# Performance work log

Measured on AMD Instinct MI355X. Metric: run time of the kernel, lower is better.

Reference implementation:

```python
import jax, jax.numpy as jnp
import numpy as np

B, S, D, UNITS = 4, 512, 256, 128
NEG = -1e9


def setup_inputs() -> dict:
    key = jax.random.key(0)
    k1, k2, k3, k4 = jax.random.split(key, 4)
    values = jax.random.normal(k1, (B, S, D), dtype=jnp.float32)
    Wq = jax.random.normal(k2, (D, UNITS), dtype=jnp.float32) * (1.0 / np.sqrt(D))
    Wv = jax.random.normal(k3, (D, UNITS), dtype=jnp.float32) * (1.0 / np.sqrt(D))
    Vw = jax.random.normal(k4, (UNITS,), dtype=jnp.float32) * (1.0 / np.sqrt(UNITS))
    return {"values": values, "Wq": Wq, "Wv": Wv, "Vw": Vw}


def reference(values, Wq, Wv, Vw):
    # values: [B, S, D]
    query = values @ Wq            # [B, S, U]
    value = values @ Wv            # [B, S, U]
    # additive (Bahdanau) score: V . tanh(q_i + v_j) -> [B, S, S]
    feat = jnp.tanh(query[:, :, None, :] + value[:, None, :, :])  # [B,S,S,U]
    score = jnp.einsum('biju,u->bij', feat, Vw)
    seq_len = values.shape[1]
    causal = jnp.tril(jnp.ones((seq_len, seq_len), dtype=jnp.float32))  # lower-tri = visible
    score = score + (1.0 - causal)[None, :, :] * jnp.asarray(NEG, score.dtype)
    attn = jax.nn.softmax(score, axis=-1)          # [B, S, S]
    context = jnp.matmul(attn, values)             # [B, S, D]
    return context
```

## Files before the change

kernel.cpp:

```cpp
#include <hip/hip_runtime.h>
#include <hip/hip_fp16.h>

#define SEQ 512
#define DIM 256
#define UN  128
#define BSZ 2048
#define CSC 2.8853900817779268f
#define EVS 2176
#define VTS 2176
#define PS  640

typedef _Float16 half8 __attribute__((ext_vector_type(8)));
typedef float   float4v __attribute__((ext_vector_type(4)));
struct h4s { __half2 a, b; };

static __device__ __forceinline__ unsigned short f2bf(float x) {
  unsigned u = __float_as_uint(x);
  u += 0x7FFF + ((u >> 16) & 1);
  return (unsigned short)(u >> 16);
}
static __device__ __forceinline__ float bf2f(unsigned short s) {
  return __uint_as_float((unsigned)s << 16);
}
static __device__ __forceinline__ float rdlane(float v, int k) {
  return __int_as_float(__builtin_amdgcn_readlane(__float_as_int(v), k));
}

__global__ __launch_bounds__(256) void proj_kernel(
    const float* __restrict__ values, const float* __restrict__ Wq,
    const float* __restrict__ Wv, float* __restrict__ Eq,
    unsigned short* __restrict__ Ev, _Float16* __restrict__ Vt) {
  __shared__ float vsm[4 * DIM];
  const int t = threadIdx.x;
  const int r0 = blockIdx.x * 4;
  {
    const int row = t >> 6, c4 = (t & 63) * 4;
    const float4 v = *(const float4*)(values + (r0 + row) * DIM + c4);
    *(float4*)&vsm[row * DIM + c4] = v;
  }
  __syncthreads();
  {
    h4s o;
    o.a = __floats2half2_rn(vsm[0 * DIM + t], vsm[1 * DIM + t]);
    o.b = __floats2half2_rn(vsm[2 * DIM + t], vsm[3 * DIM + t]);
    *(h4s*)(Vt + (size_t)t * VTS + r0) = o;
  }
  const int half = t >> 7, u = t & 127;
  const float* __restrict__ W = half ? Wv : Wq;
  float acc[4] = {0.f, 0.f, 0.f, 0.f};
  for (int d = 0; d < DIM; d += 4) {
    const float w0 = W[(d + 0) * UN + u], w1 = W[(d + 1) * UN + u];
    const float w2 = W[(d + 2) * UN + u], w3 = W[(d + 3) * UN + u];
#pragma unroll
    for (int k = 0; k < 4; ++k) {
      const float4 v = *(const float4*)&vsm[k * DIM + d];
      acc[k] = fmaf(v.x, w0, acc[k]);
      acc[k] = fmaf(v.y, w1, acc[k]);
      acc[k] = fmaf(v.z, w2, acc[k]);
      acc[k] = fmaf(v.w, w3, acc[k]);
    }
  }
  if (!half) {
#pragma unroll
    for (int k = 0; k < 4; ++k)
      Eq[(r0 + k) * UN + u] = __builtin_amdgcn_exp2f(acc[k] * CSC);
  } else {
    ushort4 o;
    o.x = f2bf(__builtin_amdgcn_exp2f(acc[0] * CSC));
    o.y = f2bf(__builtin_amdgcn_exp2f(acc[1] * CSC));
    o.z = f2bf(__builtin_amdgcn_exp2f(acc[2] * CSC));
    o.w = f2bf(__builtin_amdgcn_exp2f(acc[3] * CSC));
    *(ushort4*)(Ev + (size_t)u * EVS + r0) = o;
  }
}

__global__ __launch_bounds__(256, 4) void score_kernel(
    const float* __restrict__ Eq, const unsigned short* __restrict__ Ev,
    const float* __restrict__ Vw, _Float16* __restrict__ P) {
  __shared__ float sc[2 * SEQ];
  __shared__ float scp[2 * SEQ];
  __shared__ float invs[2];

  const int t = threadIdx.x;
  const int x = blockIdx.x;
  const int b = x >> 8, p = x & 255;
  const int bS = b * SEQ;
  const int i = p;
  const int ihi = SEQ - 1 - p;
  const int jhi = ihi;

  const float* __restrict__ eql = Eq + (size_t)(bS + i) * UN;
  const float* __restrict__ eqh = Eq + (size_t)(bS + ihi) * UN;

  {
    const int flip = ((x ^ (x >> 1) ^ (x >> 8)) & 1) << 6;
    const int tt = t ^ flip;
    const int lane = t & 63;
    const int qd = tt & 127, jb = qd << 2;
    const int u0 = (tt >> 7) << 6;
    float* __restrict__ so = (tt >> 7) ? scp : sc;
    const unsigned short* __restrict__ evp = Ev + (size_t)u0 * EVS + bS + jb;
    const float qhv = eqh[u0 + lane];
    const float qlv = eql[u0 + lane];
    const float wvv = Vw[u0 + lane];
#define LDE(K) (*(const ushort4*)(evp + (size_t)(K) * EVS))
    if ((tt & 64) == 0) {
      float h0=0.f,h1=0.f,h2=0.f,h3=0.f,l0=0.f,l1=0.f,l2=0.f,l3=0.f;
      ushort4 e[4] = {LDE(0), LDE(1), LDE(2), LDE(3)};
#pragma clang loop unroll(disable)
      for (int k = 0; k < 64; k += 4) {
#pragma unroll
        for (int r = 0; r < 4; ++r) {
          const ushort4 n = LDE(k + 4 + r);
          const float qh = rdlane(qhv, k + r);
          const float ql = rdlane(qlv, k + r);
          const float ww = rdlane(wvv, k + r);
          const float f0 = bf2f(e[r].x), f1 = bf2f(e[r].y);
          const float f2 = bf2f(e[r].z), f3 = bf2f(e[r].w);
          const float a0 = fmaf(ql, f0, 1.f), b0 = fmaf(qh, f0, 1.f);
          const float a1 = fmaf(ql, f1, 1.f), b1 = fmaf(qh, f1, 1.f);
          const float a2 = fmaf(ql, f2, 1.f), b2 = fmaf(qh, f2, 1.f);
          const float a3 = fmaf(ql, f3, 1.f), b3 = fmaf(qh, f3, 1.f);
          const float s0 = ww * __builtin_amdgcn_rcpf(a0 * b0);
          const float s1 = ww * __builtin_amdgcn_rcpf(a1 * b1);
          const float s2 = ww * __builtin_amdgcn_rcpf(a2 * b2);
          const float s3 = ww * __builtin_amdgcn_rcpf(a3 * b3);
          l0 = fmaf(s0, b0, l0); h0 = fmaf(s0, a0, h0);
          l1 = fmaf(s1, b1, l1); h1 = fmaf(s1, a1, h1);
          l2 = fmaf(s2, b2, l2); h2 = fmaf(s2, a2, h2);
          l3 = fmaf(s3, b3, l3); h3 = fmaf(s3, a3, h3);
          e[r] = n;
        }
      }
      *(float4*)&so[SEQ + jb] = make_float4(h0, h1, h2, h3);
      *(float4*)&so[jb]       = make_float4(l0, l1, l2, l3);
    } else if (jb <= jhi) {
      float h0=0.f,h1=0.f,h2=0.f,h3=0.f;
      ushort4 e[4] = {LDE(0), LDE(1), LDE(2), LDE(3)};
#pragma clang loop unroll(disable)
      for (int k = 0; k < 64; k += 4) {
#pragma unroll
        for (int r = 0; r < 4; ++r) {
          const ushort4 n = LDE(k + 4 + r);
          const float q  = rdlane(qhv, k + r);
          const float ww = rdlane(wvv, k + r);
          const float f0 = bf2f(e[r].x), f1 = bf2f(e[r].y);
          const float f2 = bf2f(e[r].z), f3 = bf2f(e[r].w);
          const float a  = fmaf(q, f0, 1.f), bb = fmaf(q, f1, 1.f);
          const float c  = fmaf(q, f2, 1.f), d  = fmaf(q, f3, 1.f);
          const float sA = ww * __builtin_amdgcn_rcpf(a * bb);
          const float sB = ww * __builtin_amdgcn_rcpf(c * d);
          h0 = fmaf(sA, bb, h0); h1 = fmaf(sA, a, h1);
          h2 = fmaf(sB, d,  h2); h3 = fmaf(sB, c, h3);
          e[r] = n;
        }
      }
      *(float4*)&so[SEQ + jb] = make_float4(h0, h1, h2, h3);
    }
#undef LDE
  }
  __syncthreads();

  {
    const int w = t >> 6, l = t & 63;
    if (w < 2) {
      const int jmax = (w == 0) ? i : jhi;
      float* __restrict__ r0p = sc + w * SEQ;
      const float* __restrict__ r1p = scp + w * SEQ;
      float m = 1e30f;
      for (int j = l; j <= jmax; j += 64) m = fminf(m, r0p[j] + r1p[j]);
#pragma unroll
      for (int o = 32; o; o >>= 1) m = fminf(m, __shfl_xor(m, o));
      float sum = 0.f;
      for (int j = l; j <= jmax; j += 64) {
        const float pr = __builtin_amdgcn_exp2f((m - (r0p[j] + r1p[j])) * CSC);
        r0p[j] = pr;
        sum += pr;
      }
#pragma unroll
      for (int o = 32; o; o >>= 1) sum += __shfl_xor(sum, o);
      if (l == 0) invs[w] = __builtin_amdgcn_rcpf(sum);
    }
  }
  __syncthreads();

  {
    const float invLo = invs[0], invHi = invs[1];
    const int t2 = t + 256;
    const float pLo = (t <= i) ? sc[t] * invLo : 0.f;
    const float pHa = sc[SEQ + t] * invHi;
    const float pHb = (t2 <= jhi) ? sc[SEQ + t2] * invHi : 0.f;
    P[(size_t)(bS + i) * PS + t]    = (_Float16)pLo;
    P[(size_t)(bS + ihi) * PS + t]  = (_Float16)pHa;
    P[(size_t)(bS + ihi) * PS + t2] = (_Float16)pHb;
  }
}

__global__ __launch_bounds__(256) void ctx_kernel(
    const _Float16* __restrict__ P, const _Float16* __restrict__ Vt,
    float* __restrict__ out) {
  const int t = threadIdx.x, lane = t & 63, g = t >> 6;
  const int x = blockIdx.x;
  const int b = x >> 7, ri = (x >> 2) & 31, cg = x & 3;
  const int bS = b * SEQ;
  const int d0 = cg * 64 + g * 16;
  const int m = lane & 15, q = lane >> 4;
  const int Kmax = 16 * ri + 16;

  const _Float16* __restrict__ pA = P  + (size_t)(bS + 16 * ri + m) * PS + q * 8;
  const _Float16* __restrict__ pB = Vt + (size_t)(d0 + m) * VTS + bS + q * 8;
  float4v acc = {0.f, 0.f, 0.f, 0.f};
  for (int k0 = 0; k0 < Kmax; k0 += 32) {
    const half8 a  = *(const half8*)(pA + k0);
    const half8 bv = *(const half8*)(pB + k0);
    acc = __builtin_amdgcn_mfma_f32_16x16x32_f16(a, bv, acc, 0, 0, 0);
  }
  float* __restrict__ o = out + (size_t)(bS + 16 * ri + q * 4) * DIM + d0 + m;
#pragma unroll
  for (int r = 0; r < 4; ++r) o[(size_t)r * DIM] = acc[r];
}

extern "C" void kernel_launch(void* const* d_in, const int* in_sizes, int n_in,
                              void* d_out, int out_size, void* d_ws, size_t ws_size,
                              hipStream_t stream) {
  const float* values = (const float*)d_in[0];
  const float* Wq     = (const float*)d_in[1];
  const float* Wv     = (const float*)d_in[2];
  const float* Vw     = (const float*)d_in[3];
  float* out = (float*)d_out;
  float* Eq = (float*)d_ws;
  unsigned short* Ev = (unsigned short*)(Eq + (size_t)BSZ * UN);
  _Float16* Vt = (_Float16*)(Ev + (size_t)136 * EVS);
  _Float16* P  = Vt + (size_t)DIM * VTS;
  proj_kernel<<<dim3(BSZ / 4), 256, 0, stream>>>(values, Wq, Wv, Eq, Ev, Vt);
  score_kernel<<<dim3(4 * 256), 256, 0, stream>>>(Eq, Ev, Vw, P);
  ctx_kernel<<<dim3(4 * 32 * 4), 256, 0, stream>>>(P, Vt, out);
}
```

Before: 99.71 us.

## Split score and softmax into separate kernels with finer score parallelism

Restructures the score stage so each block handles half the key range and waves split the unit dimension, reducing partials via shared memory and writing raw scores to a global buffer. A new softmax kernel reads rows, applies the causal mask, normalizes, and writes fp16 probabilities. This removes the serialized, mostly idle softmax phase inside the score kernel and raises occupancy, at the cost of an extra launch, a global round trip for scores, and some wasted computation on masked columns.

```diff
diff --git a/kernel.cpp b/kernel.cpp
--- a/kernel.cpp
+++ b/kernel.cpp
@@ -74,126 +74,120 @@
   }
 }
 
-__global__ __launch_bounds__(256, 4) void score_kernel(
+__global__ __launch_bounds__(256, 8) void score2_kernel(
     const float* __restrict__ Eq, const unsigned short* __restrict__ Ev,
-    const float* __restrict__ Vw, _Float16* __restrict__ P) {
-  __shared__ float sc[2 * SEQ];
-  __shared__ float scp[2 * SEQ];
-  __shared__ float invs[2];
-
-  const int t = threadIdx.x;
+    const float* __restrict__ Vw, float* __restrict__ Sd) {
+  __shared__ float pl[4 * 256];
+  __shared__ float ph[4 * 256];
+  const int t = threadIdx.x, lane = t & 63, w = t >> 6;
   const int x = blockIdx.x;
-  const int b = x >> 8, p = x & 255;
+  const int pairIdx = x >> 1, jhalf = x & 1;
+  const int b = pairIdx >> 8, p = pairIdx & 255;
   const int bS = b * SEQ;
-  const int i = p;
-  const int ihi = SEQ - 1 - p;
-  const int jhi = ihi;
-
-  const float* __restrict__ eql = Eq + (size_t)(bS + i) * UN;
-  const float* __restrict__ eqh = Eq + (size_t)(bS + ihi) * UN;
-
-  {
-    const int flip = ((x ^ (x >> 1) ^ (x >> 8)) & 1) << 6;
-    const int tt = t ^ flip;
-    const int lane = t & 63;
-    const int qd = tt & 127, jb = qd << 2;
-    const int u0 = (tt >> 7) << 6;
-    float* __restrict__ so = (tt >> 7) ? scp : sc;
-    const unsigned short* __restrict__ evp = Ev + (size_t)u0 * EVS + bS + jb;
-    const float qhv = eqh[u0 + lane];
-    const float qlv = eql[u0 + lane];
-    const float wvv = Vw[u0 + lane];
+  const int i = p, ihi = SEQ - 1 - p;
+  const int u0 = w << 5;
+  const int jb = lane << 2;
+
+  const int lk = lane & 31;
+  const float qlv = Eq[(size_t)(bS + i) * UN + u0 + lk];
+  const float qhv = Eq[(size_t)(bS + ihi) * UN + u0 + lk];
+  const float wvv = Vw[u0 + lk];
+
+  const unsigned short* __restrict__ evp =
+      Ev + (size_t)u0 * EVS + bS + (jhalf << 8) + jb;
 #define LDE(K) (*(const ushort4*)(evp + (size_t)(K) * EVS))
-    if ((tt & 64) == 0) {
-      float h0=0.f,h1=0.f,h2=0.f,h3=0.f,l0=0.f,l1=0.f,l2=0.f,l3=0.f;
-      ushort4 e[4] = {LDE(0), LDE(1), LDE(2), LDE(3)};
+  if (jhalf == 0) {
+    float h0=0.f,h1=0.f,h2=0.f,h3=0.f,l0=0.f,l1=0.f,l2=0.f,l3=0.f;
+    ushort4 e[4] = {LDE(0), LDE(1), LDE(2), LDE(3)};
 #pragma clang loop unroll(disable)
-      for (int k = 0; k < 64; k += 4) {
-#pragma unroll
-        for (int r = 0; r < 4; ++r) {
-          const ushort4 n = LDE(k + 4 + r);
-          const float qh = rdlane(qhv, k + r);
-          const float ql = rdlane(qlv, k + r);
-          const float ww = rdlane(wvv, k + r);
-          const float f0 = bf2f(e[r].x), f1 = bf2f(e[r].y);
-          const float f2 = bf2f(e[r].z), f3 = bf2f(e[r].w);
-          const float a0 = fmaf(ql, f0, 1.f), b0 = fmaf(qh, f0, 1.f);
-          const float a1 = fmaf(ql, f1, 1.f), b1 = fmaf(qh, f1, 1.f);
-          const float a2 = fmaf(ql, f2, 1.f), b2 = fmaf(qh, f2, 1.f);
-          const float a3 = fmaf(ql, f3, 1.f), b3 = fmaf(qh, f3, 1.f);
-          const float s0 = ww * __builtin_amdgcn_rcpf(a0 * b0);
-          const float s1 = ww * __builtin_amdgcn_rcpf(a1 * b1);
-          const float s2 = ww * __builtin_amdgcn_rcpf(a2 * b2);
-          const float s3 = ww * __builtin_amdgcn_rcpf(a3 * b3);
-          l0 = fmaf(s0, b0, l0); h0 = fmaf(s0, a0, h0);
-          l1 = fmaf(s1, b1, l1); h1 = fmaf(s1, a1, h1);
-          l2 = fmaf(s2, b2, l2); h2 = fmaf(s2, a2, h2);
-          l3 = fmaf(s3, b3, l3); h3 = fmaf(s3, a3, h3);
-          e[r] = n;
-        }
+    for (int k = 0; k < 32; k += 4) {
+#pragma unroll
+      for (int r = 0; r < 4; ++r) {
+        const ushort4 n = LDE(k + 4 + r);
+        const float qh = rdlane(qhv, k + r);
+        const float ql = rdlane(qlv, k + r);
+        const float ww = rdlane(wvv, k + r);
+        const float f0 = bf2f(e[r].x), f1 = bf2f(e[r].y);
+        const float f2 = bf2f(e[r].z), f3 = bf2f(e[r].w);
+        const float a0 = fmaf(ql, f0, 1.f), b0 = fmaf(qh, f0, 1.f);
+        const float a1 = fmaf(ql, f1, 1.f), b1 = fmaf(qh, f1, 1.f);
+        const float a2 = fmaf(ql, f2, 1.f), b2 = fmaf(qh, f2, 1.f);
+        const float a3 = fmaf(ql, f3, 1.f), b3 = fmaf(qh, f3, 1.f);
+        const float s0 = ww * __builtin_amdgcn_rcpf(a0 * b0);
+        const float s1 = ww * __builtin_amdgcn_rcpf(a1 * b1);
+        const float s2 = ww * __builtin_amdgcn_rcpf(a2 * b2);
+        const float s3 = ww * __builtin_amdgcn_rcpf(a3 * b3);
+        l0 = fmaf(s0, b0, l0); h0 = fmaf(s0, a0, h0);
+        l1 = fmaf(s1, b1, l1); h1 = fmaf(s1, a1, h1);
+        l2 = fmaf(s2, b2, l2); h2 = fmaf(s2, a2, h2);
+        l3 = fmaf(s3, b3, l3); h3 = fmaf(s3, a3, h3);
+        e[r] = n;
       }
-      *(float4*)&so[SEQ + jb] = make_float4(h0, h1, h2, h3);
-      *(float4*)&so[jb]       = make_float4(l0, l1, l2, l3);
-    } else if (jb <= jhi) {
-      float h0=0.f,h1=0.f,h2=0.f,h3=0.f;
-      ushort4 e[4] = {LDE(0), LDE(1), LDE(2), LDE(3)};
+    }
+    *(float4*)&pl[(w << 8) + jb] = make_float4(l0, l1, l2, l3);
+    *(float4*)&ph[(w << 8) + jb] = make_float4(h0, h1, h2, h3);
+    __syncthreads();
+    const float lo = pl[t] + pl[256 + t] + pl[512 + t] + pl[768 + t];
+    const float hi = ph[t] + ph[256 + t] + ph[512 + t] + ph[768 + t];
+    Sd[(size_t)(bS + i) * SEQ + t]   = lo;
+    Sd[(size_t)(bS + ihi) * SEQ + t] = hi;
+  } else {
+    float h0=0.f,h1=0.f,h2=0.f,h3=0.f;
+    ushort4 e[4] = {LDE(0), LDE(1), LDE(2), LDE(3)};
 #pragma clang loop unroll(disable)
-      for (int k = 0; k < 64; k += 4) {
-#pragma unroll
-        for (int r = 0; r < 4; ++r) {
-          const ushort4 n = LDE(k + 4 + r);
-          const float q  = rdlane(qhv, k + r);
-          const float ww = rdlane(wvv, k + r);
-          const float f0 = bf2f(e[r].x), f1 = bf2f(e[r].y);
-          const float f2 = bf2f(e[r].z), f3 = bf2f(e[r].w);
-          const float a  = fmaf(q, f0, 1.f), bb = fmaf(q, f1, 1.f);
-          const float c  = fmaf(q, f2, 1.f), d  = fmaf(q, f3, 1.f);
-          const float sA = ww * __builtin_amdgcn_rcpf(a * bb);
-          const float sB = ww * __builtin_amdgcn_rcpf(c * d);
-          h0 = fmaf(sA, bb, h0); h1 = fmaf(sA, a, h1);
-          h2 = fmaf(sB, d,  h2); h3 = fmaf(sB, c, h3);
-          e[r] = n;
-        }
+    for (int k = 0; k < 32; k += 4) {
+#pragma unroll
+      for (int r = 0; r < 4; ++r) {
+        const ushort4 n = LDE(k + 4 + r);
+        const float qh = rdlane(qhv, k + r);
+        const float ww = rdlane(wvv, k + r);
+        const float f0 = bf2f(e[r].x), f1 = bf2f(e[r].y);
+        const float f2 = bf2f(e[r].z), f3 = bf2f(e[r].w);
+        const float a  = fmaf(qh, f0, 1.f), bb = fmaf(qh, f1, 1.f);
+        const float c  = fmaf(qh, f2, 1.f), d  = fmaf(qh, f3, 1.f);
+        const float sA = ww * __builtin_amdgcn_rcpf(a * bb);
+        const float sB = ww * __builtin_amdgcn_rcpf(c * d);
+        h0 = fmaf(sA, bb, h0); h1 = fmaf(sA, a, h1);
+        h2 = fmaf(sB, d,  h2); h3 = fmaf(sB, c, h3);
+        e[r] = n;
       }
-      *(float4*)&so[SEQ + jb] = make_float4(h0, h1, h2, h3);
     }
+    *(float4*)&ph[(w << 8) + jb] = make_float4(h0, h1, h2, h3);
+    __syncthreads();
+    const float hi = ph[t] + ph[256 + t] + ph[512 + t] + ph[768 + t];
+    Sd[(size_t)(bS + ihi) * SEQ + 256 + t] = hi;
+  }
 #undef LDE
-  }
-  __syncthreads();
-
-  {
-    const int w = t >> 6, l = t & 63;
-    if (w < 2) {
-      const int jmax = (w == 0) ? i : jhi;
-      float* __restrict__ r0p = sc + w * SEQ;
-      const float* __restrict__ r1p = scp + w * SEQ;
-      float m = 1e30f;
-      for (int j = l; j <= jmax; j += 64) m = fminf(m, r0p[j] + r1p[j]);
-#pragma unroll
-      for (int o = 32; o; o >>= 1) m = fminf(m, __shfl_xor(m, o));
-      float sum = 0.f;
-      for (int j = l; j <= jmax; j += 64) {
-        const float pr = __builtin_amdgcn_exp2f((m - (r0p[j] + r1p[j])) * CSC);
-        r0p[j] = pr;
-        sum += pr;
-      }
-#pragma unroll
-      for (int o = 32; o; o >>= 1) sum += __shfl_xor(sum, o);
-      if (l == 0) invs[w] = __builtin_amdgcn_rcpf(sum);
-    }
-  }
-  __syncthreads();
-
-  {
-    const float invLo = invs[0], invHi = invs[1];
-    const int t2 = t + 256;
-    const float pLo = (t <= i) ? sc[t] * invLo : 0.f;
-    const float pHa = sc[SEQ + t] * invHi;
-    const float pHb = (t2 <= jhi) ? sc[SEQ + t2] * invHi : 0.f;
-    P[(size_t)(bS + i) * PS + t]    = (_Float16)pLo;
-    P[(size_t)(bS + ihi) * PS + t]  = (_Float16)pHa;
-    P[(size_t)(bS + ihi) * PS + t2] = (_Float16)pHb;
-  }
+}
+
+__global__ __launch_bounds__(256) void smax_kernel(
+    const float* __restrict__ Sd, _Float16* __restrict__ P) {
+  const int t = threadIdx.x, lane = t & 63, w = t >> 6;
+  const int r = blockIdx.x * 4 + w;
+  const int i = r & (SEQ - 1);
+  const float* __restrict__ row = Sd + (size_t)r * SEQ;
+  const int c0 = lane * 8;
+  const float4 sA = *(const float4*)(row + c0);
+  const float4 sB = *(const float4*)(row + c0 + 4);
+  float v[8] = {sA.x, sA.y, sA.z, sA.w, sB.x, sB.y, sB.z, sB.w};
+  float m = 1e30f;
+#pragma unroll
+  for (int c = 0; c < 8; ++c) if (c0 + c <= i) m = fminf(m, v[c]);
+#pragma unroll
+  for (int o = 32; o; o >>= 1) m = fminf(m, __shfl_xor(m, o));
+  float pr[8]; float sum = 0.f;
+#pragma unroll
+  for (int c = 0; c < 8; ++c) {
+    pr[c] = (c0 + c <= i) ? __builtin_amdgcn_exp2f((m - v[c]) * CSC) : 0.f;
+    sum += pr[c];
+  }
+#pragma unroll
+  for (int o = 32; o; o >>= 1) sum += __shfl_xor(sum, o);
+  const float inv = __builtin_amdgcn_rcpf(sum);
+  half8 o8;
+#pragma unroll
+  for (int c = 0; c < 8; ++c) o8[c] = (_Float16)(pr[c] * inv);
+  *(half8*)(P + (size_t)r * PS + c0) = o8;
 }
 
 __global__ __launch_bounds__(256) void ctx_kernel(
@@ -232,7 +226,9 @@
   unsigned short* Ev = (unsigned short*)(Eq + (size_t)BSZ * UN);
   _Float16* Vt = (_Float16*)(Ev + (size_t)136 * EVS);
   _Float16* P  = Vt + (size_t)DIM * VTS;
+  float* Sd    = (float*)(P + (size_t)BSZ * PS);
   proj_kernel<<<dim3(BSZ / 4), 256, 0, stream>>>(values, Wq, Wv, Eq, Ev, Vt);
-  score_kernel<<<dim3(4 * 256), 256, 0, stream>>>(Eq, Ev, Vw, P);
-  ctx_kernel<<<dim3(4 * 32 * 4), 256, 0, stream>>>(P, Vt, out);
-}
+  score2_kernel<<<dim3(2048), 256, 0, stream>>>(Eq, Ev, Vw, Sd);
+  smax_kernel<<<dim3(512), 256, 0, stream>>>(Sd, P);
+  ctx_kernel<<<dim3(512), 256, 0, stream>>>(P, Vt, out);
+}
```

Result: no change. 100.8 us (+1.1%).

## Split score units four ways and give each lane eight contiguous columns

Applied to the files above, without the earlier changes.

Restructures the score kernel so each of the four waves handles 32 units across all 512 columns, with each lane holding eight columns via 16-byte bf16 loads. Partial scores go to per-wave shared buffers and are summed across the four waves during the softmax pass. This uses wider loads and removes the divergent lo/hi thread split. In exchange, every lane now computes both row scores for all columns, including lower-row columns past 256 that are discarded and upper-row columns beyond the causal limit, so arithmetic per block rises.

```diff
diff --git a/kernel.cpp b/kernel.cpp
--- a/kernel.cpp
+++ b/kernel.cpp
@@ -12,6 +12,7 @@
 
 typedef _Float16 half8 __attribute__((ext_vector_type(8)));
 typedef float   float4v __attribute__((ext_vector_type(4)));
+typedef unsigned short us8 __attribute__((ext_vector_type(8)));
 struct h4s { __half2 a, b; };
 
 static __device__ __forceinline__ unsigned short f2bf(float x) {
@@ -77,109 +78,107 @@
 __global__ __launch_bounds__(256, 4) void score_kernel(
     const float* __restrict__ Eq, const unsigned short* __restrict__ Ev,
     const float* __restrict__ Vw, _Float16* __restrict__ P) {
-  __shared__ float sc[2 * SEQ];
-  __shared__ float scp[2 * SEQ];
+  __shared__ float shi4[4 * SEQ];
+  __shared__ float slo4[4 * 256];
   __shared__ float invs[2];
 
-  const int t = threadIdx.x;
+  const int t = threadIdx.x, lane = t & 63, w = t >> 6;
   const int x = blockIdx.x;
   const int b = x >> 8, p = x & 255;
   const int bS = b * SEQ;
   const int i = p;
   const int ihi = SEQ - 1 - p;
   const int jhi = ihi;
-
-  const float* __restrict__ eql = Eq + (size_t)(bS + i) * UN;
-  const float* __restrict__ eqh = Eq + (size_t)(bS + ihi) * UN;
-
-  {
-    const int flip = ((x ^ (x >> 1) ^ (x >> 8)) & 1) << 6;
-    const int tt = t ^ flip;
-    const int lane = t & 63;
-    const int qd = tt & 127, jb = qd << 2;
-    const int u0 = (tt >> 7) << 6;
-    float* __restrict__ so = (tt >> 7) ? scp : sc;
-    const unsigned short* __restrict__ evp = Ev + (size_t)u0 * EVS + bS + jb;
-    const float qhv = eqh[u0 + lane];
-    const float qlv = eql[u0 + lane];
-    const float wvv = Vw[u0 + lane];
-#define LDE(K) (*(const ushort4*)(evp + (size_t)(K) * EVS))
-    if ((tt & 64) == 0) {
-      float h0=0.f,h1=0.f,h2=0.f,h3=0.f,l0=0.f,l1=0.f,l2=0.f,l3=0.f;
-      ushort4 e[4] = {LDE(0), LDE(1), LDE(2), LDE(3)};
+  const int u0 = w << 5;
+  const int lk = lane & 31;
+
+  const float qlv = Eq[(size_t)(bS + i) * UN + u0 + lk];
+  const float qhv = Eq[(size_t)(bS + ihi) * UN + u0 + lk];
+  const float wvv = Vw[u0 + lk];
+
+  {
+    const unsigned short* __restrict__ evp = Ev + (size_t)u0 * EVS + bS + lane * 8;
+#define LDE(K) (*(const us8*)(evp + (size_t)(K) * EVS))
+    float h[8], l[8];
+#pragma unroll
+    for (int c = 0; c < 8; ++c) { h[c] = 0.f; l[c] = 0.f; }
+    us8 e0 = LDE(0), e1 = LDE(1);
 #pragma clang loop unroll(disable)
-      for (int k = 0; k < 64; k += 4) {
-#pragma unroll
-        for (int r = 0; r < 4; ++r) {
-          const ushort4 n = LDE(k + 4 + r);
-          const float qh = rdlane(qhv, k + r);
-          const float ql = rdlane(qlv, k + r);
-          const float ww = rdlane(wvv, k + r);
-          const float f0 = bf2f(e[r].x), f1 = bf2f(e[r].y);
-          const float f2 = bf2f(e[r].z), f3 = bf2f(e[r].w);
-          const float a0 = fmaf(ql, f0, 1.f), b0 = fmaf(qh, f0, 1.f);
-          const float a1 = fmaf(ql, f1, 1.f), b1 = fmaf(qh, f1, 1.f);
-          const float a2 = fmaf(ql, f2, 1.f), b2 = fmaf(qh, f2, 1.f);
-          const float a3 = fmaf(ql, f3, 1.f), b3 = fmaf(qh, f3, 1.f);
-          const float s0 = ww * __builtin_amdgcn_rcpf(a0 * b0);
-          const float s1 = ww * __builtin_amdgcn_rcpf(a1 * b1);
-          const float s2 = ww * __builtin_amdgcn_rcpf(a2 * b2);
-          const float s3 = ww * __builtin_amdgcn_rcpf(a3 * b3);
-          l0 = fmaf(s0, b0, l0); h0 = fmaf(s0, a0, h0);
-          l1 = fmaf(s1, b1, l1); h1 = fmaf(s1, a1, h1);
-          l2 = fmaf(s2, b2, l2); h2 = fmaf(s2, a2, h2);
-          l3 = fmaf(s3, b3, l3); h3 = fmaf(s3, a3, h3);
-          e[r] = n;
+    for (int k = 0; k < 32; k += 2) {
+      {
+        const us8 n = LDE(k + 2);
+        const float qh = rdlane(qhv, k), ql = rdlane(qlv, k), ww = rdlane(wvv, k);
+#pragma unroll
+        for (int c = 0; c < 8; ++c) {
+          const float f = bf2f(e0[c]);
+          const float aa = fmaf(ql, f, 1.f);
+          const float bb = fmaf(qh, f, 1.f);
+          const float s = ww * __builtin_amdgcn_rcpf(aa * bb);
+          l[c] = fmaf(s, bb, l[c]);
+          h[c] = fmaf(s, aa, h[c]);
         }
-      }
-      *(float4*)&so[SEQ + jb] = make_float4(h0, h1, h2, h3);
-      *(float4*)&so[jb]       = make_float4(l0, l1, l2, l3);
-    } else if (jb <= jhi) {
-      float h0=0.f,h1=0.f,h2=0.f,h3=0.f;
-      ushort4 e[4] = {LDE(0), LDE(1), LDE(2), LDE(3)};
-#pragma clang loop unroll(disable)
-      for (int k = 0; k < 64; k += 4) {
-#pragma unroll
-        for (int r = 0; r < 4; ++r) {
-          const ushort4 n = LDE(k + 4 + r);
-          const float q  = rdlane(qhv, k + r);
-          const float ww = rdlane(wvv, k + r);
-          const float f0 = bf2f(e[r].x), f1 = bf2f(e[r].y);
-          const float f2 = bf2f(e[r].z), f3 = bf2f(e[r].w);
-          const float a  = fmaf(q, f0, 1.f), bb = fmaf(q, f1, 1.f);
-          const float c  = fmaf(q, f2, 1.f), d  = fmaf(q, f3, 1.f);
-          const float sA = ww * __builtin_amdgcn_rcpf(a * bb);
-          const float sB = ww * __builtin_amdgcn_rcpf(c * d);
-          h0 = fmaf(sA, bb, h0); h1 = fmaf(sA, a, h1);
-          h2 = fmaf(sB, d,  h2); h3 = fmaf(sB, c, h3);
-          e[r] = n;
+        e0 = n;
+      }
+      {
+        const us8 n = LDE(k + 3);
+        const float qh = rdlane(qhv, k + 1), ql = rdlane(qlv, k + 1), ww = rdlane(wvv, k + 1);
+#pragma unroll
+        for (int c = 0; c < 8; ++c) {
+          const float f = bf2f(e1[c]);
+          const float aa = fmaf(ql, f, 1.f);
+          const float bb = fmaf(qh, f, 1.f);
+          const float s = ww * __builtin_amdgcn_rcpf(aa * bb);
+          l[c] = fmaf(s, bb, l[c]);
+          h[c] = fmaf(s, aa, h[c]);
         }
-      }
-      *(float4*)&so[SEQ + jb] = make_float4(h0, h1, h2, h3);
+        e1 = n;
+      }
     }
 #undef LDE
+    float* __restrict__ hw = &shi4[(w << 9) + lane * 8];
+    *(float4*)(hw + 0) = make_float4(h[0], h[1], h[2], h[3]);
+    *(float4*)(hw + 4) = make_float4(h[4], h[5], h[6], h[7]);
+    if (lane < 32) {
+      float* __restrict__ lw = &slo4[(w << 8) + lane * 8];
+      *(float4*)(lw + 0) = make_float4(l[0], l[1], l[2], l[3]);
+      *(float4*)(lw + 4) = make_float4(l[4], l[5], l[6], l[7]);
+    }
   }
   __syncthreads();
 
   {
-    const int w = t >> 6, l = t & 63;
-    if (w < 2) {
-      const int jmax = (w == 0) ? i : jhi;
-      float* __restrict__ r0p = sc + w * SEQ;
-      const float* __restrict__ r1p = scp + w * SEQ;
+    if (w == 0) {
       float m = 1e30f;
-      for (int j = l; j <= jmax; j += 64) m = fminf(m, r0p[j] + r1p[j]);
+      for (int j = lane; j <= i; j += 64)
+        m = fminf(m, slo4[j] + slo4[256 + j] + slo4[512 + j] + slo4[768 + j]);
 #pragma unroll
       for (int o = 32; o; o >>= 1) m = fminf(m, __shfl_xor(m, o));
       float sum = 0.f;
-      for (int j = l; j <= jmax; j += 64) {
-        const float pr = __builtin_amdgcn_exp2f((m - (r0p[j] + r1p[j])) * CSC);
-        r0p[j] = pr;
+      for (int j = lane; j <= i; j += 64) {
+        const float s = slo4[j] + slo4[256 + j] + slo4[512 + j] + slo4[768 + j];
+        const float pr = __builtin_amdgcn_exp2f((m - s) * CSC);
+        slo4[j] = pr;
         sum += pr;
       }
 #pragma unroll
       for (int o = 32; o; o >>= 1) sum += __shfl_xor(sum, o);
-      if (l == 0) invs[w] = __builtin_amdgcn_rcpf(sum);
+      if (lane == 0) invs[0] = __builtin_amdgcn_rcpf(sum);
+    } else if (w == 1) {
+      float m = 1e30f;
+      for (int j = lane; j <= jhi; j += 64)
+        m = fminf(m, shi4[j] + shi4[512 + j] + shi4[1024 + j] + shi4[1536 + j]);
+#pragma unroll
+      for (int o = 32; o; o >>= 1) m = fminf(m, __shfl_xor(m, o));
+      float sum = 0.f;
+      for (int j = lane; j <= jhi; j += 64) {
+        const float s = shi4[j] + shi4[512 + j] + shi4[1024 + j] + shi4[1536 + j];
+        const float pr = __builtin_amdgcn_exp2f((m - s) * CSC);
+        shi4[j] = pr;
+        sum += pr;
+      }
+#pragma unroll
+      for (int o = 32; o; o >>= 1) sum += __shfl_xor(sum, o);
+      if (lane == 0) invs[1] = __builtin_amdgcn_rcpf(sum);
     }
   }
   __syncthreads();
@@ -187,9 +186,9 @@
   {
     const float invLo = invs[0], invHi = invs[1];
     const int t2 = t + 256;
-    const float pLo = (t <= i) ? sc[t] * invLo : 0.f;
-    const float pHa = sc[SEQ + t] * invHi;
-    const float pHb = (t2 <= jhi) ? sc[SEQ + t2] * invHi : 0.f;
+    const float pLo = (t <= i) ? slo4[t] * invLo : 0.f;
+    const float pHa = shi4[t] * invHi;
+    const float pHb = (t2 <= jhi) ? shi4[t2] * invHi : 0.f;
     P[(size_t)(bS + i) * PS + t]    = (_Float16)pLo;
     P[(size_t)(bS + ihi) * PS + t]  = (_Float16)pHa;
     P[(size_t)(bS + ihi) * PS + t2] = (_Float16)pHb;
@@ -234,5 +233,5 @@
   _Float16* P  = Vt + (size_t)DIM * VTS;
   proj_kernel<<<dim3(BSZ / 4), 256, 0, stream>>>(values, Wq, Wv, Eq, Ev, Vt);
   score_kernel<<<dim3(4 * 256), 256, 0, stream>>>(Eq, Ev, Vw, P);
-  ctx_kernel<<<dim3(4 * 32 * 4), 256, 0, stream>>>(P, Vt, out);
-}
+  ctx_kernel<<<dim3(512), 256, 0, stream>>>(P, Vt, out);
+}
```

Result: no change. 97.85 us (-1.9%).
